# Kernel optimization log

Hardware: AMD Instinct MI355X
Metric: run time of the kernel (lower is better)

## Reference

```python
import jax, jax.numpy as jnp
import numpy as np

# ---- module config (matches init_kwargs) ----
OGFH, OGFW = 256, 704
DOWNSAMPLE = 8
FH, FW = OGFH // DOWNSAMPLE, OGFW // DOWNSAMPLE   # 32, 88
DBOUND = (4.0, 45.0, 1.0)
D = int((DBOUND[1] - DBOUND[0]) / DBOUND[2])      # 41 depth bins
CAMC = 64
XB = (-50.0, 50.0, 0.5)    # lateral  -> nx = 200
YB = (-10.0, 10.0, 20.0)   # vertical -> ny = 1
ZB = (0.0, 50.0, 0.25)     # depth    -> nz = 200
NX = np.array([int((b[1] - b[0]) / b[2]) for b in (XB, YB, ZB)])  # [200, 1, 200]
DX = np.array([b[2] for b in (XB, YB, ZB)], dtype=np.float32)
BX = np.array([b[0] + b[2] / 2.0 for b in (XB, YB, ZB)], dtype=np.float32)


def make_frustum():
    # matches create_frustum_1camera: [D, fH, fW, 3] of (u, v, depth)
    ds = jnp.broadcast_to(
        jnp.arange(DBOUND[0], DBOUND[1], DBOUND[2], dtype=jnp.float32)[:, None, None],
        (D, FH, FW))
    xs = jnp.broadcast_to(
        jnp.linspace(0.0, OGFW - 1, FW, dtype=jnp.float32)[None, None, :], (D, FH, FW))
    ys = jnp.broadcast_to(
        jnp.linspace(0.0, OGFH - 1, FH, dtype=jnp.float32)[None, :, None], (D, FH, FW))
    return jnp.stack((xs, ys, ds), -1)


def setup_inputs() -> dict:
    key = jax.random.key(0)
    B = 4
    # depthnet output: first D channels = depth logits, next CAMC = context feats
    x = jax.random.normal(key, (B, D + CAMC, FH, FW), dtype=jnp.float32)
    fx = fy = 520.0
    K = jnp.array([[fx, 0.0, OGFW / 2.0],
                   [0.0, fy, OGFH / 2.0],
                   [0.0, 0.0, 1.0]], dtype=jnp.float32)
    intrins = jnp.broadcast_to(K, (B, 3, 3))
    post_rots = jnp.broadcast_to(jnp.eye(3, dtype=jnp.float32), (B, 3, 3))
    post_trans = jnp.zeros((B, 3), dtype=jnp.float32)
    return {"x": x, "intrins": intrins, "post_rots": post_rots, "post_trans": post_trans}


def _forward(x, intrins, post_rots, post_trans):
    B = x.shape[0]
    frustum = make_frustum()                                                     # [D,H,W,3]
    # ---- get_geometry ----
    pts = frustum[None] - post_trans[:, None, None, None, :]                     # [B,D,H,W,3]
    pts = jnp.einsum('bij,bdhwj->bdhwi', jnp.linalg.inv(post_rots), pts)
    pts = jnp.concatenate([pts[..., :2] * pts[..., 2:3], pts[..., 2:3]], -1)     # un-normalize
    geom = jnp.einsum('bij,bdhwj->bdhwi', jnp.linalg.inv(intrins), pts)          # [B,D,H,W,3]
    # ---- lift: depth softmax (x) context features ----
    depth = jax.nn.softmax(x[:, :D], axis=1)                                     # [B,D,H,W]
    feat = x[:, D:D + CAMC]                                                      # [B,C,H,W]
    vol = depth[:, None] * feat[:, :, None]                                      # [B,C,D,H,W]
    vol = jnp.transpose(vol, (0, 2, 3, 4, 1))                                    # [B,D,H,W,C]
    # ---- voxel_splat (sort+cumsum trick == segmented sum) ----
    Nprime = B * D * FH * FW
    feats = vol.reshape(Nprime, CAMC)
    # torch .long() truncates toward zero -> astype(int32)
    coords = ((geom - (BX - DX / 2.0)) / DX).astype(jnp.int32).reshape(Nprime, 3)
    bix = jnp.repeat(jnp.arange(B, dtype=jnp.int32), Nprime // B)
    kept = ((coords[:, 0] >= 0) & (coords[:, 0] < int(NX[0])) &
            (coords[:, 1] >= 0) & (coords[:, 1] < int(NX[1])) &
            (coords[:, 2] >= 0) & (coords[:, 2] < int(NX[2])))
    nseg = int(NX[0] * NX[1] * NX[2]) * B
    ranks = (coords[:, 0] * (int(NX[1]) * int(NX[2]) * B)
             + coords[:, 1] * (int(NX[2]) * B)
             + coords[:, 2] * B + bix)
    ranks = jnp.where(kept, ranks, nseg)  # dump bucket for dropped points
    pooled = jax.ops.segment_sum(jnp.where(kept[:, None], feats, 0.0), ranks,
                                 num_segments=nseg + 1)[:nseg]
    final = pooled.reshape(int(NX[0]), int(NX[1]), int(NX[2]), B, CAMC)          # [x,y,z,B,C]
    final = jnp.transpose(final, (3, 4, 1, 2, 0))                                # [B,C,ny,nz,nx]
    # torch.cat(final.unbind(dim=2), 1): collapse ny into channels (y-major)
    final = jnp.transpose(final, (0, 2, 1, 3, 4)).reshape(
        B, CAMC * int(NX[1]), int(NX[2]), int(NX[0]))                            # [B,C,200,200]
    return final


def reference(x, intrins, post_rots, post_trans):
    return _forward(x, intrins, post_rots, post_trans)
```

## Files before the change

kernel.cpp:

```cpp
#include <hip/hip_runtime.h>
#include <math.h>

#define DD   41
#define FHh  32
#define FWw  88
#define CC   64
#define CH   32
#define CG8  8
#define NXx  200
#define NZz  200
#define NCH  (DD + CC)
#define PLANE ((size_t)FHh * FWw)
#define NE   (DD * FWw)
#define DCAP 4
#define OVCAP 4096

__global__ __launch_bounds__(256) void lss_colpool(
    const float* __restrict__ x,
    const float* __restrict__ intrins,
    const float* __restrict__ post_rots,
    const float* __restrict__ post_trans,
    float* __restrict__ P, int* __restrict__ V,
    int* __restrict__ rowcnt8, int* __restrict__ ovcnt)
{
    __shared__ float Wt[DD][FHh + 1];
    __shared__ float F4s[FHh][36];
    __shared__ float Mi[18];
    __shared__ float pm[8][FHh + 1];
    __shared__ int   Vtmp[DD];

    int blk   = blockIdx.x;
    int chalf = blk & 1;
    int w     = (blk >> 1) % FWw;
    int b     = blk / (2 * FWw);
    int t     = threadIdx.x;
    const float* xb = x + (size_t)b * NCH * PLANE + w;

    for (int idx = t; idx < DD * FHh; idx += 256) {
        int d = idx >> 5, h = idx & 31;
        Wt[d][h] = xb[((size_t)d * FHh + h) * FWw];
    }
    for (int idx = t; idx < FHh * CH; idx += 256) {
        int c = idx & 31, h = idx >> 5;
        F4s[h][c] = xb[((size_t)(DD + chalf * CH + c) * FHh + h) * FWw];
    }
    if (t >= 64 && t < 64 + DD) Vtmp[t - 64] = -1;
    if (t == 0) {
        #pragma clang fp contract(off)
        for (int m = 0; m < 2; ++m) {
            const float* A = (m == 0 ? post_rots : intrins) + b * 9;
            float* O = Mi + m * 9;
            float a = A[0], bb = A[1], c = A[2];
            float d = A[3], e  = A[4], f = A[5];
            float g = A[6], h  = A[7], i = A[8];
            float det = a * (e * i - f * h) - bb * (d * i - f * g) + c * (d * h - e * g);
            O[0] = (e * i - f * h) / det;
            O[1] = (c * h - bb * i) / det;
            O[2] = (bb * f - c * e) / det;
            O[3] = (f * g - d * i) / det;
            O[4] = (a * i - c * g) / det;
            O[5] = (c * d - a * f) / det;
            O[6] = (d * h - e * g) / det;
            O[7] = (bb * g - a * h) / det;
            O[8] = (a * e - bb * d) / det;
        }
    }
    __syncthreads();

    int h = t & 31, l = t >> 5;
    float e_[6];
    {
        float pmax = -INFINITY;
        for (int d = l; d < DD; d += 8) pmax = fmaxf(pmax, Wt[d][h]);
        pm[l][h] = pmax;
    }
    __syncthreads();
    float mx = -INFINITY;
    for (int j = 0; j < 8; ++j) mx = fmaxf(mx, pm[j][h]);
    __syncthreads();
    {
        #pragma clang fp contract(off)
        float psum = 0.0f;
        int k = 0;
        for (int d = l; d < DD; d += 8, ++k) {
            float e = expf(Wt[d][h] - mx);
            e_[k] = e; psum += e;
        }
        pm[l][h] = psum;
    }
    __syncthreads();
    float s = 0.0f;
    for (int j = 0; j < 8; ++j) s += pm[j][h];

    {
        #pragma clang fp contract(off)
        float xs = (float)((double)w * 703.0 / 87.0);
        float ys = (float)((double)h * 255.0 / 31.0);
        float tx = post_trans[b * 3 + 0];
        float ty = post_trans[b * 3 + 1];
        float tz = post_trans[b * 3 + 2];
        int k = 0;
        for (int d = l; d < DD; d += 8, ++k) {
            float z  = 4.0f + (float)d;
            float px = xs - tx, py = ys - ty, pz = z - tz;
            float rx = Mi[0] * px + Mi[1] * py + Mi[2] * pz;
            float ry = Mi[3] * px + Mi[4] * py + Mi[5] * pz;
            float rz = Mi[6] * px + Mi[7] * py + Mi[8] * pz;
            float qx = rx * rz, qy = ry * rz, qz = rz;
            float gx = Mi[ 9] * qx + Mi[10] * qy + Mi[11] * qz;
            float gy = Mi[12] * qx + Mi[13] * qy + Mi[14] * qz;
            float gz = Mi[15] * qx + Mi[16] * qy + Mi[17] * qz;
            float cx = (gx + 50.0f) / 0.5f;
            float cy = (gy + 10.0f) / 20.0f;
            float cz = gz / 0.25f;
            int ix = (int)cx;
            int iy = (int)cy;
            int iz = (int)cz;
            bool kept = (ix >= 0) & (ix < NXx) & (iy == 0) & (iz >= 0) & (iz < NZz);
            if (kept) {
                Wt[d][h] = e_[k] / s;
                Vtmp[d] = iz * NXx + ix;
            } else {
                Wt[d][h] = 0.0f;
            }
        }
    }
    __syncthreads();

    float* Pb = P + ((size_t)b * NE) * CC + chalf * CH;
    {
        int c4 = t & 7;
        for (int d = t >> 3; d < DD; d += 32) {
            float4 acc = make_float4(0.f, 0.f, 0.f, 0.f);
            for (int hh = 0; hh < FHh; ++hh) {
                float wtv = Wt[d][hh];
                float4 fv = *(const float4*)&F4s[hh][c4 * 4];
                acc.x += wtv * fv.x; acc.y += wtv * fv.y;
                acc.z += wtv * fv.z; acc.w += wtv * fv.w;
            }
            *(float4*)&Pb[((size_t)d * FWw + w) * CC + c4 * 4] = acc;
        }
    }
    if (chalf == 0) {
        if (t < DD) V[(size_t)b * NE + (size_t)t * FWw + w] = Vtmp[t];
        if (w == 0) for (int i = t; i < NZz * 8; i += 256) rowcnt8[b * NZz * 8 + i] = 0;
    }
    if (blk == 0 && t == 0) *ovcnt = 0;
}

__global__ __launch_bounds__(256) void lss_rowbuild(
    const float* __restrict__ P, const int* __restrict__ V,
    float* __restrict__ S, int* __restrict__ izd,
    int* __restrict__ rowcnt8, int* __restrict__ dlist8,
    int* __restrict__ ovcnt, int* __restrict__ ovlist,
    float* __restrict__ out)
{
    __shared__ float acc[CG8 * (NXx + 1)];
    __shared__ int ixw[FWw];
    __shared__ int izw[FWw];
    __shared__ int key;
    __shared__ int s_k;

    int blk = blockIdx.x;
    int cg = blk & 7;
    int bd = blk >> 3;
    int d = bd % DD;
    int b = bd / DD;
    int t = threadIdx.x;

    if (t == 0) key = 0x7fffffff;
    for (int i = t; i < CG8 * (NXx + 1); i += 256) acc[i] = 0.0f;
    __syncthreads();
    if (t < FWw) {
        int v = V[(size_t)bd * FWw + t];
        if (v >= 0) {
            int iz = v / NXx;
            izw[t] = iz; ixw[t] = v - iz * NXx;
            atomicMin(&key, (t << 16) | iz);
        } else { izw[t] = -1; ixw[t] = -1; }
    }
    __syncthreads();
    int kk = key;
    int s_iz = (kk == 0x7fffffff) ? -1 : (kk & 0xffff);
    if (cg == 0 && t == 0) izd[bd] = s_iz;
    if (s_iz < 0) return;

    int r = b * NZz + s_iz;
    if (t == 0) {
        int k = atomicAdd(&rowcnt8[r * 8 + cg], 1);
        if (k < DCAP) dlist8[(r * 8 + cg) * DCAP + k] = d;
        s_k = k;
    }
    if (cg == 0 && t < FWw && izw[t] >= 0 && izw[t] != s_iz) {
        int k = atomicAdd(ovcnt, 1);
        if (k < OVCAP)
            ovlist[k] = (b << 29) | (d << 23) | (t << 16) | (ixw[t] << 8) | izw[t];
    }

    const float* Pb = P + (size_t)bd * FWw * CC + cg * CG8;
    for (int idx = t; idx < FWw * 2; idx += 256) {
        int w = idx >> 1, q = idx & 1;
        if (izw[w] == s_iz) {
            float4 v = *(const float4*)&Pb[(size_t)w * CC + q * 4];
            int ix = ixw[w];
            int cb = q * 4;
            atomicAdd(&acc[(cb + 0) * (NXx + 1) + ix], v.x);
            atomicAdd(&acc[(cb + 1) * (NXx + 1) + ix], v.y);
            atomicAdd(&acc[(cb + 2) * (NXx + 1) + ix], v.z);
            atomicAdd(&acc[(cb + 3) * (NXx + 1) + ix], v.w);
        }
    }
    __syncthreads();

    bool owner0 = (s_k == 0);
    for (int i = t; i < CG8 * (NXx / 4); i += 256) {
        int c = i / (NXx / 4), q = i - c * (NXx / 4);
        int base = c * (NXx + 1) + q * 4;
        float4 vv;
        vv.x = acc[base + 0];
        vv.y = acc[base + 1];
        vv.z = acc[base + 2];
        vv.w = acc[base + 3];
        if (owner0) {
            float* orow = out + (((size_t)(b * CC + cg * CG8 + c)) * NZz + s_iz) * NXx;
            ((float4*)orow)[q] = vv;
        } else {
            float* Srow = S + ((size_t)bd * CC + cg * CG8 + c) * NXx;
            ((float4*)Srow)[q] = vv;
        }
    }
}

__global__ __launch_bounds__(256) void lss_writeout(
    const float* __restrict__ S, const int* __restrict__ izd,
    const int* __restrict__ rowcnt8, const int* __restrict__ dlist8,
    const float* __restrict__ P,
    const int* __restrict__ ovcnt, const int* __restrict__ ovlist,
    float* __restrict__ out)
{
    __shared__ int s_n[50];
    __shared__ int s_d[50 * DCAP];

    int blk = blockIdx.x;
    int qz = blk & 3;
    int bc = blk >> 2;
    int c  = bc % CC;
    int b  = bc / CC;
    int cg = c >> 3;
    int iz0 = qz * 50;
    int t = threadIdx.x;

    for (int i = t; i < 50; i += 256)
        s_n[i] = rowcnt8[(b * NZz + iz0 + i) * 8 + cg];
    for (int i = t; i < 50 * DCAP; i += 256) {
        int row = i / DCAP, k = i - row * DCAP;
        s_d[i] = dlist8[((b * NZz + iz0 + row) * 8 + cg) * DCAP + k];
    }
    __syncthreads();

    float* obase = out + (((size_t)b * CC + c) * NZz + iz0) * NXx;
    const float* Sb = S + (size_t)b * DD * CC * NXx;

    for (int i = t; i < 50 * (NXx / 4); i += 256) {
        int izl = i / (NXx / 4), q = i - izl * (NXx / 4);
        int n = s_n[izl];
        if (n == 1) continue;
        float4 vv = make_float4(0.f, 0.f, 0.f, 0.f);
        if (n > 1) {
            float4 cur = ((float4*)obase)[i];
            vv.x += cur.x; vv.y += cur.y; vv.z += cur.z; vv.w += cur.w;
            if (n <= DCAP) {
                for (int k = 1; k < n; ++k) {
                    int d = s_d[izl * DCAP + k];
                    float4 sv = ((const float4*)(Sb + ((size_t)d * CC + c) * NXx))[q];
                    vv.x += sv.x; vv.y += sv.y; vv.z += sv.z; vv.w += sv.w;
                }
            } else {
                int iz = iz0 + izl;
                int owner0 = s_d[izl * DCAP + 0];
                for (int d = 0; d < DD; ++d) {
                    if (izd[b * DD + d] == iz && d != owner0) {
                        float4 sv = ((const float4*)(Sb + ((size_t)d * CC + c) * NXx))[q];
                        vv.x += sv.x; vv.y += sv.y; vv.z += sv.z; vv.w += sv.w;
                    }
                }
            }
        }
        ((float4*)obase)[i] = vv;
    }

    int nov = *ovcnt;
    if (nov > 0) {
        __syncthreads();
        if (t == 0) {
            if (nov > OVCAP) nov = OVCAP;
            for (int k = 0; k < nov; ++k) {
                int ent = ovlist[k];
                int eb  = (ent >> 29) & 7;
                int ed  = (ent >> 23) & 63;
                int ew  = (ent >> 16) & 127;
                int eix = (ent >> 8) & 255;
                int eiz = ent & 255;
                if (eb == b && eiz >= iz0 && eiz < iz0 + 50) {
                    size_t o = (((size_t)b * CC + c) * NZz + eiz) * NXx + eix;
                    out[o] += P[(((size_t)eb * DD + ed) * FWw + ew) * CC + c];
                }
            }
        }
    }
}

extern "C" void kernel_launch(void* const* d_in, const int* in_sizes, int n_in,
                              void* d_out, int out_size, void* d_ws, size_t ws_size,
                              hipStream_t stream)
{
    const float* x          = (const float*)d_in[0];
    const float* intrins    = (const float*)d_in[1];
    const float* post_rots  = (const float*)d_in[2];
    const float* post_trans = (const float*)d_in[3];
    float* out = (float*)d_out;

    int B = in_sizes[0] / (NCH * (int)PLANE);

    size_t off = 0;
    auto alloc = [&](size_t bytes) {
        void* p = (char*)d_ws + off;
        off = (off + bytes + 255) & ~(size_t)255;
        return p;
    };
    float* P       = (float*)alloc((size_t)B * NE * CC * sizeof(float));
    int*   V       = (int*)  alloc((size_t)B * NE * sizeof(int));
    float* S       = (float*)alloc((size_t)B * DD * CC * NXx * sizeof(float));
    int*   izd     = (int*)  alloc((size_t)B * DD * sizeof(int));
    int*   rowcnt8 = (int*)  alloc((size_t)B * NZz * 8 * sizeof(int));
    int*   dlist8  = (int*)  alloc((size_t)B * NZz * 8 * DCAP * sizeof(int));
    int*   ovcnt   = (int*)  alloc(256);
    int*   ovlist  = (int*)  alloc((size_t)OVCAP * sizeof(int));

    lss_colpool<<<B * FWw * 2, 256, 0, stream>>>(x, intrins, post_rots, post_trans,
                                                 P, V, rowcnt8, ovcnt);
    lss_rowbuild<<<B * DD * 8, 256, 0, stream>>>(P, V, S, izd, rowcnt8, dlist8,
                                                 ovcnt, ovlist, out);
    lss_writeout<<<B * CC * 4, 256, 0, stream>>>(S, izd, rowcnt8, dlist8, P,
                                                 ovcnt, ovlist, out);
}
```

Before: 100.9 us.

## Zero output in colpool and replace full writeout pass with sparse atomic fixup

New measurement: 99.60 us. No clear change (-1.3%).

```diff
diff --git a/kernel.cpp b/kernel.cpp
--- a/kernel.cpp
+++ b/kernel.cpp
@@ -21,7 +21,8 @@
     const float* __restrict__ post_rots,
     const float* __restrict__ post_trans,
     float* __restrict__ P, int* __restrict__ V,
-    int* __restrict__ rowcnt8, int* __restrict__ ovcnt)
+    int* __restrict__ rowcnt8, int* __restrict__ ovcnt,
+    float* __restrict__ out, int out_quads)
 {
     __shared__ float Wt[DD][FHh + 1];
     __shared__ float F4s[FHh][36];
@@ -146,6 +147,13 @@
         if (w == 0) for (int i = t; i < NZz * 8; i += 256) rowcnt8[b * NZz * 8 + i] = 0;
     }
     if (blk == 0 && t == 0) *ovcnt = 0;
+
+    {
+        float4 z = make_float4(0.f, 0.f, 0.f, 0.f);
+        float4* o4 = (float4*)out;
+        int stride = gridDim.x * 256;
+        for (int i = blk * 256 + t; i < out_quads; i += stride) o4[i] = z;
+    }
 }
 
 __global__ __launch_bounds__(256) void lss_rowbuild(
@@ -231,80 +239,57 @@
     }
 }
 
-__global__ __launch_bounds__(256) void lss_writeout(
+__global__ __launch_bounds__(256) void lss_fixup(
     const float* __restrict__ S, const int* __restrict__ izd,
     const int* __restrict__ rowcnt8, const int* __restrict__ dlist8,
     const float* __restrict__ P,
     const int* __restrict__ ovcnt, const int* __restrict__ ovlist,
     float* __restrict__ out)
 {
-    __shared__ int s_n[50];
-    __shared__ int s_d[50 * DCAP];
-
-    int blk = blockIdx.x;
-    int qz = blk & 3;
-    int bc = blk >> 2;
-    int c  = bc % CC;
-    int b  = bc / CC;
-    int cg = c >> 3;
-    int iz0 = qz * 50;
+    int b = blockIdx.x;
     int t = threadIdx.x;
 
-    for (int i = t; i < 50; i += 256)
-        s_n[i] = rowcnt8[(b * NZz + iz0 + i) * 8 + cg];
-    for (int i = t; i < 50 * DCAP; i += 256) {
-        int row = i / DCAP, k = i - row * DCAP;
-        s_d[i] = dlist8[((b * NZz + iz0 + row) * 8 + cg) * DCAP + k];
-    }
-    __syncthreads();
-
-    float* obase = out + (((size_t)b * CC + c) * NZz + iz0) * NXx;
-    const float* Sb = S + (size_t)b * DD * CC * NXx;
-
-    for (int i = t; i < 50 * (NXx / 4); i += 256) {
-        int izl = i / (NXx / 4), q = i - izl * (NXx / 4);
-        int n = s_n[izl];
-        if (n == 1) continue;
-        float4 vv = make_float4(0.f, 0.f, 0.f, 0.f);
-        if (n > 1) {
-            float4 cur = ((float4*)obase)[i];
-            vv.x += cur.x; vv.y += cur.y; vv.z += cur.z; vv.w += cur.w;
-            if (n <= DCAP) {
-                for (int k = 1; k < n; ++k) {
-                    int d = s_d[izl * DCAP + k];
-                    float4 sv = ((const float4*)(Sb + ((size_t)d * CC + c) * NXx))[q];
-                    vv.x += sv.x; vv.y += sv.y; vv.z += sv.z; vv.w += sv.w;
+    for (int pair = t; pair < NZz * 8; pair += 256) {
+        int n = rowcnt8[b * NZz * 8 + pair];
+        if (n <= 1) continue;
+        int iz = pair >> 3, cg = pair & 7;
+        const int* dl = dlist8 + (size_t)(b * NZz * 8 + pair) * DCAP;
+        if (n <= DCAP) {
+            for (int k = 1; k < n; ++k) {
+                int d = dl[k];
+                for (int c = 0; c < CG8; ++c) {
+                    const float* Srow = S + ((size_t)(b * DD + d) * CC + cg * CG8 + c) * NXx;
+                    float* orow = out + (((size_t)(b * CC + cg * CG8 + c)) * NZz + iz) * NXx;
+                    for (int ix = 0; ix < NXx; ++ix) atomicAdd(&orow[ix], Srow[ix]);
                 }
-            } else {
-                int iz = iz0 + izl;
-                int owner0 = s_d[izl * DCAP + 0];
-                for (int d = 0; d < DD; ++d) {
-                    if (izd[b * DD + d] == iz && d != owner0) {
-                        float4 sv = ((const float4*)(Sb + ((size_t)d * CC + c) * NXx))[q];
-                        vv.x += sv.x; vv.y += sv.y; vv.z += sv.z; vv.w += sv.w;
+            }
+        } else {
+            int owner0 = dl[0];
+            for (int d = 0; d < DD; ++d) {
+                if (izd[b * DD + d] == iz && d != owner0) {
+                    for (int c = 0; c < CG8; ++c) {
+                        const float* Srow = S + ((size_t)(b * DD + d) * CC + cg * CG8 + c) * NXx;
+                        float* orow = out + (((size_t)(b * CC + cg * CG8 + c)) * NZz + iz) * NXx;
+                        for (int ix = 0; ix < NXx; ++ix) atomicAdd(&orow[ix], Srow[ix]);
                     }
                 }
             }
         }
-        ((float4*)obase)[i] = vv;
-    }
-
-    int nov = *ovcnt;
-    if (nov > 0) {
-        __syncthreads();
-        if (t == 0) {
-            if (nov > OVCAP) nov = OVCAP;
-            for (int k = 0; k < nov; ++k) {
-                int ent = ovlist[k];
-                int eb  = (ent >> 29) & 7;
-                int ed  = (ent >> 23) & 63;
-                int ew  = (ent >> 16) & 127;
-                int eix = (ent >> 8) & 255;
-                int eiz = ent & 255;
-                if (eb == b && eiz >= iz0 && eiz < iz0 + 50) {
-                    size_t o = (((size_t)b * CC + c) * NZz + eiz) * NXx + eix;
-                    out[o] += P[(((size_t)eb * DD + ed) * FWw + ew) * CC + c];
-                }
+    }
+
+    if (b == 0 && t == 0) {
+        int nov = *ovcnt;
+        if (nov > OVCAP) nov = OVCAP;
+        for (int k = 0; k < nov; ++k) {
+            int ent = ovlist[k];
+            int eb  = (ent >> 29) & 7;
+            int ed  = (ent >> 23) & 63;
+            int ew  = (ent >> 16) & 127;
+            int eix = (ent >> 8) & 255;
+            int eiz = ent & 255;
+            for (int c = 0; c < CC; ++c) {
+                size_t o = (((size_t)(eb * CC + c)) * NZz + eiz) * NXx + eix;
+                atomicAdd(&out[o], P[(((size_t)eb * DD + ed) * FWw + ew) * CC + c]);
             }
         }
     }
@@ -337,10 +322,11 @@
     int*   ovcnt   = (int*)  alloc(256);
     int*   ovlist  = (int*)  alloc((size_t)OVCAP * sizeof(int));
 
+    int out_quads = out_size / 4;
+
     lss_colpool<<<B * FWw * 2, 256, 0, stream>>>(x, intrins, post_rots, post_trans,
-                                                 P, V, rowcnt8, ovcnt);
+                                                 P, V, rowcnt8, ovcnt, out, out_quads);
     lss_rowbuild<<<B * DD * 8, 256, 0, stream>>>(P, V, S, izd, rowcnt8, dlist8,
                                                  ovcnt, ovlist, out);
-    lss_writeout<<<B * CC * 4, 256, 0, stream>>>(S, izd, rowcnt8, dlist8, P,
-                                                 ovcnt, ovlist, out);
+    lss_fixup<<<B, 256, 0, stream>>>(S, izd, rowcnt8, dlist8, P, ovcnt, ovlist, out);
 }
```
